# Performance work log

Hardware: AMD Instinct MI355X
Metric: run time of the kernel (lower is better)

Reference implementation:

```python
import jax, jax.numpy as jnp
import numpy as np

N, E, IN = 50000, 800000, 128   # nodes, edges, input feature dim
H, C = 8, 32                    # heads, per-head channels
HC = H * C                      # 256 = concat width
NEG_SLOPE = 0.2
BN_EPS = 1e-5


def _gat_conv(x, src, dst, W, a_src, a_dst, b, heads, out_ch, concat):
    """PyG-style GATConv (eval mode, self-loops already in src/dst)."""
    n = x.shape[0]
    h = (x @ W).reshape(n, heads, out_ch)                 # [N,H,C]
    alpha_s = (h * a_src).sum(-1)                         # [N,H]
    alpha_d = (h * a_dst).sum(-1)                         # [N,H]
    e = jax.nn.leaky_relu(alpha_s[src] + alpha_d[dst], NEG_SLOPE)  # [Etot,H]
    # segment softmax over destination nodes (every node has a self-loop)
    emax = jax.ops.segment_max(e, dst, num_segments=n)    # [N,H]
    e = jnp.exp(e - emax[dst])
    denom = jax.ops.segment_sum(e, dst, num_segments=n)
    alpha = e / (denom[dst] + 1e-16)                      # [Etot,H]
    msg = h[src] * alpha[:, :, None]                      # [Etot,H,C]
    out = jax.ops.segment_sum(msg, dst, num_segments=n)   # [N,H,C]
    out = out.reshape(n, heads * out_ch) if concat else out.mean(axis=1)
    return out + b


def _bn(y, g, beta, m, v):
    return (y - m) * jax.lax.rsqrt(v + BN_EPS) * g + beta


def setup_inputs() -> dict:
    key = jax.random.key(0)
    ks = jax.random.split(key, 32)
    def p(i, shape, s=0.1):
        return jax.random.normal(ks[i], shape, dtype=jnp.float32) * s
    x = jax.random.normal(ks[0], (N, IN), dtype=jnp.float32)
    edge_index = jax.random.randint(ks[1], (2, E), 0, N, dtype=jnp.int32)
    d = dict(
        x=x, edge_index=edge_index,
        W1=p(2, (IN, HC)), a_src1=p(3, (H, C)), a_dst1=p(4, (H, C)), b1=p(5, (HC,)),
        bn1_g=jnp.ones((HC,), jnp.float32), bn1_b=jnp.zeros((HC,), jnp.float32),
        bn1_m=p(6, (HC,)), bn1_v=jax.random.uniform(ks[7], (HC,), jnp.float32, 0.5, 1.5),
        W2=p(8, (HC, HC)), a_src2=p(9, (H, C)), a_dst2=p(10, (H, C)), b2=p(11, (HC,)),
        bn2_g=jnp.ones((HC,), jnp.float32), bn2_b=jnp.zeros((HC,), jnp.float32),
        bn2_m=p(12, (HC,)), bn2_v=jax.random.uniform(ks[13], (HC,), jnp.float32, 0.5, 1.5),
        W3=p(14, (HC, C)), a_src3=p(15, (1, C)), a_dst3=p(16, (1, C)), b3=p(17, (C,)),
        Ws1=p(18, (IN, HC)), bs1=p(19, (HC,)),
        Ws2=p(20, (HC, C)), bs2=p(21, (C,)),
    )
    return d


def reference(x, edge_index, W1, a_src1, a_dst1, b1, bn1_g, bn1_b, bn1_m, bn1_v,
              W2, a_src2, a_dst2, b2, bn2_g, bn2_b, bn2_m, bn2_v,
              W3, a_src3, a_dst3, b3, Ws1, bs1, Ws2, bs2):
    n = x.shape[0]
    loops = jnp.arange(n, dtype=edge_index.dtype)
    src = jnp.concatenate([edge_index[0], loops])   # PyG add_self_loops=True
    dst = jnp.concatenate([edge_index[1], loops])
    x0 = x @ Ws1 + bs1                               # skip1
    h = _gat_conv(x, src, dst, W1, a_src1, a_dst1, b1, H, C, True)
    h = jax.nn.elu(_bn(h, bn1_g, bn1_b, bn1_m, bn1_v)) + x0
    xs = h @ Ws2 + bs2                               # skip2
    h2 = _gat_conv(h, src, dst, W2, a_src2, a_dst2, b2, H, C, True)
    h2 = jax.nn.elu(_bn(h2, bn2_g, bn2_b, bn2_m, bn2_v))
    out = _gat_conv(h2, src, dst, W3, a_src3, a_dst3, b3, 1, C, False) + xs
    return out
```

## Files before the change

kernel.cpp:

```cpp
#include <hip/hip_runtime.h>
#include <hip/hip_bf16.h>

#define NEG_SLOPE 0.2f
#define BN_EPS 1e-5f
#define BSH 8
#define STASH_CAP 6400

typedef __attribute__((ext_vector_type(8))) short bf16x8;
typedef __attribute__((ext_vector_type(4))) float f32x4;
typedef __attribute__((ext_vector_type(2))) float f32x2;

#if defined(__has_builtin)
#if __has_builtin(__builtin_amdgcn_cvt_f32_fp8) && __has_builtin(__builtin_amdgcn_cvt_pk_fp8_f32)
#define HW_FP8 1
#endif
#if __has_builtin(__builtin_amdgcn_cvt_pk_f32_fp8)
#define HW_FP8_PK 1
#endif
#endif

__device__ __forceinline__ float bf2f(unsigned short u) {
    union { unsigned int i; float f; } x;
    x.i = ((unsigned int)u) << 16;
    return x.f;
}
__device__ __forceinline__ unsigned short f2bf(float f) {
    __hip_bfloat16 b = __float2bfloat16(f);
    return *reinterpret_cast<unsigned short*>(&b);
}
__device__ __forceinline__ float lrelu(float v) {
    return v > 0.f ? v : NEG_SLOPE * v;
}
__device__ __forceinline__ void gload_lds16(const void* g, void* l) {
    __builtin_amdgcn_global_load_lds(
        (const __attribute__((address_space(1))) unsigned int*)(g),
        (__attribute__((address_space(3))) unsigned int*)(l),
        16, 0, 0);
}

__device__ __forceinline__ unsigned char f8enc(float f) {
#ifdef HW_FP8
    int p = __builtin_amdgcn_cvt_pk_fp8_f32(f, 0.f, 0, false);
    return (unsigned char)(p & 0xff);
#else
    float a = fabsf(f);
    unsigned int sign = (__float_as_uint(f) >> 31) << 7;
    if (a < 0.0009765625f) return (unsigned char)sign;
    a = fminf(a, 448.f);
    unsigned int bits = __float_as_uint(a);
    int e = (int)((bits >> 23) & 0xff) - 127;
    unsigned int mant = bits & 0x7fffff;
    if (e < -6) {
        int q = (int)(a * 512.f + 0.5f);
        if (q >= 8) return (unsigned char)(sign | 0x08);
        return (unsigned char)(sign | q);
    }
    unsigned int m = mant >> 20;
    unsigned int rem = mant & 0xfffff;
    if (rem > 0x80000 || (rem == 0x80000 && (m & 1))) m++;
    if (m == 8) { m = 0; e++; }
    if (e > 8) { e = 8; m = 6; }
    return (unsigned char)(sign | ((unsigned int)(e + 7) << 3) | m);
#endif
}
template <int SEL>
__device__ __forceinline__ float f8dec(unsigned int w) {
#ifdef HW_FP8
    return __builtin_amdgcn_cvt_f32_fp8(w, SEL);
#else
    unsigned int b = (w >> (SEL * 8)) & 0xff;
    unsigned int s = b >> 7, em = b & 0x7f;
    float mag;
    if (em >= 8) {
        unsigned int bits = (((em >> 3) + 120) << 23) | ((em & 7) << 20);
        mag = __uint_as_float(bits);
    } else {
        mag = (float)em * 0.001953125f;
    }
    return s ? -mag : mag;
#endif
}
__device__ __forceinline__ void fma_f8x4(float we, unsigned int wv, float4& acc) {
#ifdef HW_FP8_PK
    f32x2 lo = __builtin_amdgcn_cvt_pk_f32_fp8((int)wv, false);
    f32x2 hi = __builtin_amdgcn_cvt_pk_f32_fp8((int)wv, true);
    acc.x = fmaf(we, lo[0], acc.x);
    acc.y = fmaf(we, lo[1], acc.y);
    acc.z = fmaf(we, hi[0], acc.z);
    acc.w = fmaf(we, hi[1], acc.w);
#else
    acc.x = fmaf(we, f8dec<0>(wv), acc.x);
    acc.y = fmaf(we, f8dec<1>(wv), acc.y);
    acc.z = fmaf(we, f8dec<2>(wv), acc.z);
    acc.w = fmaf(we, f8dec<3>(wv), acc.w);
#endif
}

__device__ __forceinline__ int block_scan_incl(int v, int t) {
    int lane = t & 63, w = t >> 6;
    int sv = v;
    #pragma unroll
    for (int off = 1; off < 64; off <<= 1) {
        int u = __shfl_up(sv, off);
        if (lane >= off) sv += u;
    }
    __shared__ int ws_[4];
    if (lane == 63) ws_[w] = sv;
    __syncthreads();
    if (t == 0) {
        int a = 0;
        #pragma unroll
        for (int k = 0; k < 4; k++) { int x = ws_[k]; ws_[k] = a; a += x; }
    }
    __syncthreads();
    return sv + ws_[w];
}

__global__ __launch_bounds__(256) void phase1(const int* __restrict__ dstl,
                                              int E, int N, int NB,
                                              int* __restrict__ gHist,
                                              const float* __restrict__ x,
                                              unsigned short* __restrict__ xb, int n4x,
                                              const float* __restrict__ W1,
                                              const float* __restrict__ Ws1,
                                              const float* __restrict__ W2,
                                              const float* __restrict__ Ws2,
                                              const float* __restrict__ W3,
                                              unsigned short* __restrict__ Wcat1,
                                              unsigned short* __restrict__ Wcat2,
                                              unsigned short* __restrict__ W3t) {
    int t = threadIdx.x;
    if (blockIdx.x < 256) {
        __shared__ int h[256];
        h[t] = 0;
        __syncthreads();
        int Etot = E + N;
        for (int i = blockIdx.x * 256 + t; i < Etot; i += 256 * 256) {
            int d = (i < E) ? dstl[i] : (i - E);
            atomicAdd(&h[d >> BSH], 1);
        }
        __syncthreads();
        if (t < NB && h[t]) atomicAdd(&gHist[t], h[t]);
        return;
    }
    int i = (blockIdx.x - 256) * 256 + t;
    if (i < n4x) {
        float4 v = reinterpret_cast<const float4*>(x)[i];
        ushort4 o;
        o.x = f2bf(v.x); o.y = f2bf(v.y); o.z = f2bf(v.z); o.w = f2bf(v.w);
        reinterpret_cast<ushort4*>(xb)[i] = o;
        return;
    }
    int j = i - n4x;
    if (j < 32768) {
        int m = j >> 7, k = j & 127;
        Wcat1[j] = f2bf(W1[k * 256 + m]);
    } else if (j < 65536) {
        int q = j - 32768; int m = q >> 7, k = q & 127;
        Wcat1[32768 + q] = f2bf(Ws1[k * 256 + m]);
    } else if (j < 131072) {
        int q = j - 65536; int m = q >> 8, k = q & 255;
        Wcat2[q] = f2bf(W2[k * 256 + m]);
    } else if (j < 139264) {
        int q = j - 131072; int m = q >> 8, k = q & 255;
        Wcat2[65536 + q] = f2bf(Ws2[k * 32 + m]);
    } else if (j < 147456) {
        int q = j - 139264; int m = q >> 8, k = q & 255;
        W3t[q] = f2bf(W3[k * 32 + m]);
    }
}

__global__ __launch_bounds__(256) void bucket_scatter(const int* __restrict__ srcl,
                                                      const int* __restrict__ dstl,
                                                      int E, int N, int NB,
                                                      const int* __restrict__ gHist,
                                                      int* __restrict__ gCursor,
                                                      unsigned int* __restrict__ bktEdges) {
    __shared__ unsigned int stage[4096];
    __shared__ int lbase[256];
    __shared__ int hist[256];
    __shared__ int bexcl[257];
    __shared__ int curk[256];
    __shared__ int gbase[256];
    int t = threadIdx.x;
    int Etot = E + N;
    int begin = blockIdx.x * 4096;

    int gv = (t < NB) ? gHist[t] : 0;
    int gincl = block_scan_incl(gv, t);
    lbase[t] = gincl - gv;
    __syncthreads();

    hist[t] = 0;
    __syncthreads();

    unsigned int ent[16];
    int eb[16];
    #pragma unroll
    for (int k = 0; k < 16; k++) {
        int i = begin + k * 256 + t;
        if (i < Etot) {
            int s, d;
            if (i < E) { s = srcl[i]; d = dstl[i]; }
            else       { s = d = i - E; }
            eb[k] = d >> BSH;
            ent[k] = ((unsigned int)s << BSH) | (unsigned int)(d & 255);
            atomicAdd(&hist[eb[k]], 1);
        } else eb[k] = -1;
    }
    __syncthreads();

    int v = hist[t];
    int incl = block_scan_incl(v, t);
    bexcl[t] = incl - v;
    curk[t] = incl - v;
    if (t == 255) bexcl[256] = incl;
    __syncthreads();

    #pragma unroll
    for (int k = 0; k < 16; k++) {
        if (eb[k] >= 0) {
            int slot = atomicAdd(&curk[eb[k]], 1);
            stage[slot] = ent[k];
        }
    }
    if (t < NB) {
        int cnt = hist[t];
        gbase[t] = cnt ? (lbase[t] + atomicAdd(&gCursor[t], cnt)) : 0;
    }
    __syncthreads();

    int total = bexcl[256];
    for (int p = t; p < total; p += 256) {
        int lo = 0, hi = NB - 1;
        while (lo < hi) {
            int mid = (lo + hi + 1) >> 1;
            if (bexcl[mid] <= p) lo = mid; else hi = mid - 1;
        }
        bktEdges[gbase[lo] + (p - bexcl[lo])] = stage[p];
    }
}

__global__ __launch_bounds__(256) void bucket_to_csr(const unsigned int* __restrict__ bktEdges,
                                                     const int* __restrict__ gHist,
                                                     int* __restrict__ indptr,
                                                     int* __restrict__ esrc,
                                                     int N, int NB, int Etot) {
    __shared__ int lbase[256];
    __shared__ int nh[256];
    __shared__ int ncur[256];
    __shared__ unsigned int stash[STASH_CAP];
    int b = blockIdx.x, t = threadIdx.x;

    int gv = (t < NB) ? gHist[t] : 0;
    int gincl = block_scan_incl(gv, t);
    lbase[t] = gincl - gv;
    __syncthreads();
    int base = lbase[b];
    int cnt = gHist[b];
    int nodeBase = b << BSH;

    nh[t] = 0;
    __syncthreads();
    for (int p = t; p < cnt; p += 256) {
        unsigned int e = bktEdges[base + p];
        if (p < STASH_CAP) stash[p] = e;
        atomicAdd(&nh[e & 255], 1);
    }
    __syncthreads();
    int v = nh[t];
    int incl = block_scan_incl(v, t);
    int excl = incl - v;
    ncur[t] = excl;
    if (nodeBase + t < N) indptr[nodeBase + t] = base + excl;
    __syncthreads();
    for (int p = t; p < cnt; p += 256) {
        unsigned int e = (p < STASH_CAP) ? stash[p] : bktEdges[base + p];
        int slot = atomicAdd(&ncur[e & 255], 1);
        esrc[base + slot] = (int)(e >> BSH);
    }
    if (b == 0 && t == 0) indptr[N] = Etot;
}

__global__ __launch_bounds__(256) void gemm_tile(const unsigned short* __restrict__ A,
                                                 const unsigned short* __restrict__ Bt,
                                                 unsigned short* __restrict__ outBf,
                                                 unsigned char* __restrict__ outQ,
                                                 unsigned short* __restrict__ outSk,
                                                 const float* __restrict__ biasSk,
                                                 const float* __restrict__ aS,
                                                 const float* __restrict__ aD,
                                                 float* __restrict__ asOut,
                                                 float* __restrict__ adOut,
                                                 int M, int K, int NCtot, int split,
                                                 int ldBf, int ldSk) {
    __shared__ __align__(16) char smem[2][2][8192];
    int t = threadIdx.x;
    int w = t >> 6, lane = t & 63;
    int l16 = lane & 15, quad = lane >> 4;
    int warp_r = w >> 1, warp_c = w & 1;
    int rowBase = blockIdx.y * 128;
    int colBase = blockIdx.x * 128;

    int row_l = t & 127;
    int jchunk = t >> 7;
    int arow_st = rowBase + row_l; if (arow_st >= M) arow_st = M - 1;
    int bcol_st = colBase + row_l; if (bcol_st >= NCtot) bcol_st = NCtot - 1;
    const unsigned short* aRow = A + (size_t)arow_st * K;
    const unsigned short* bRow = Bt + (size_t)bcol_st * K;

    f32x4 acc[4][4];
    #pragma unroll
    for (int i = 0; i < 4; i++)
        #pragma unroll
        for (int j = 0; j < 4; j++) acc[i][j] = (f32x4){0.f, 0.f, 0.f, 0.f};

    auto stage = [&](int buf, int k0) {
        #pragma unroll
        for (int j = 0; j < 2; j++) {
            int chunk = j * 2 + jchunk;
            gload_lds16(aRow + k0 + chunk * 8, &smem[buf][0][(size_t)j * 4096 + (size_t)t * 16]);
            gload_lds16(bRow + k0 + chunk * 8, &smem[buf][1][(size_t)j * 4096 + (size_t)t * 16]);
        }
    };

    stage(0, 0);
    __syncthreads();
    int niter = K >> 5;
    for (int it = 0; it < niter; ++it) {
        if (it + 1 < niter) stage((it + 1) & 1, (it + 1) << 5);
        const char* Ab = &smem[it & 1][0][0];
        const char* Bb = &smem[it & 1][1][0];
        bf16x8 a[4], b[4];
        #pragma unroll
        for (int i = 0; i < 4; i++)
            a[i] = *reinterpret_cast<const bf16x8*>(Ab + quad * 2048 + (warp_r * 64 + i * 16 + l16) * 16);
        #pragma unroll
        for (int j = 0; j < 4; j++)
            b[j] = *reinterpret_cast<const bf16x8*>(Bb + quad * 2048 + (warp_c * 64 + j * 16 + l16) * 16);
        #pragma unroll
        for (int i = 0; i < 4; i++)
            #pragma unroll
            for (int j = 0; j < 4; j++)
                acc[i][j] = __builtin_amdgcn_mfma_f32_16x16x32_bf16(a[i], b[j], acc[i][j], 0, 0, 0);
        __syncthreads();
    }

    if (aS && colBase < split) {
        if (NCtot >= 128) {
            int c0 = colBase + warp_c * 64 + l16;
            int hbase = (colBase + warp_c * 64) >> 5;
            float as0 = aS[c0],      ad0 = aD[c0];
            float as1 = aS[c0 + 16], ad1 = aD[c0 + 16];
            float as2 = aS[c0 + 32], ad2 = aD[c0 + 32];
            float as3 = aS[c0 + 48], ad3 = aD[c0 + 48];
            #pragma unroll
            for (int i = 0; i < 4; i++) {
                #pragma unroll
                for (int r = 0; r < 4; r++) {
                    float va0 = acc[i][0][r] * as0 + acc[i][1][r] * as1;
                    float vd0 = acc[i][0][r] * ad0 + acc[i][1][r] * ad1;
                    float va1 = acc[i][2][r] * as2 + acc[i][3][r] * as3;
                    float vd1 = acc[i][2][r] * ad2 + acc[i][3][r] * ad3;
                    #pragma unroll
                    for (int off = 1; off < 16; off <<= 1) {
                        va0 += __shfl_xor(va0, off);
                        vd0 += __shfl_xor(vd0, off);
                        va1 += __shfl_xor(va1, off);
                        vd1 += __shfl_xor(vd1, off);
                    }
                    int row = rowBase + warp_r * 64 + i * 16 + quad * 4 + r;
                    if (l16 == 0 && row < M) {
                        asOut[row * 8 + hbase]     = va0;
                        adOut[row * 8 + hbase]     = vd0;
                        asOut[row * 8 + hbase + 1] = va1;
                        adOut[row * 8 + hbase + 1] = vd1;
                    }
                }
            }
        } else if (warp_c == 0) {
            float as0 = aS[l16],      ad0 = aD[l16];
            float as1 = aS[l16 + 16], ad1 = aD[l16 + 16];
            #pragma unroll
            for (int i = 0; i < 4; i++) {
                #pragma unroll
                for (int r = 0; r < 4; r++) {
                    float va = acc[i][0][r] * as0 + acc[i][1][r] * as1;
                    float vd = acc[i][0][r] * ad0 + acc[i][1][r] * ad1;
                    #pragma unroll
                    for (int off = 1; off < 16; off <<= 1) {
                        va += __shfl_xor(va, off);
                        vd += __shfl_xor(vd, off);
                    }
                    int row = rowBase + warp_r * 64 + i * 16 + quad * 4 + r;
                    if (l16 == 0 && row < M) {
                        asOut[row] = va;
                        adOut[row] = vd;
                    }
                }
            }
        }
    }

    #pragma unroll
    for (int i = 0; i < 4; i++) {
        #pragma unroll
        for (int r = 0; r < 4; r++) {
            int row = rowBase + warp_r * 64 + i * 16 + quad * 4 + r;
            if (row >= M) continue;
            #pragma unroll
            for (int j = 0; j < 4; j++) {
                int c = colBase + warp_c * 64 + j * 16 + l16;
                if (c >= NCtot) continue;
                float v = acc[i][j][r];
                if (c < split) {
                    if (outBf) outBf[(size_t)row * ldBf + c] = f2bf(v);
                    if (outQ)  outQ[(size_t)row * ldBf + c] = f8enc(v);
                } else {
                    outSk[(size_t)row * ldSk + (c - split)] = f2bf(v + biasSk[c - split]);
                }
            }
        }
    }
}

template <int MODE>
__global__ __launch_bounds__(256) void agg256(const unsigned char* __restrict__ hq,
                                              const float* __restrict__ as,
                                              const float* __restrict__ ad,
                                              const int* __restrict__ indptr,
                                              const int* __restrict__ esrc,
                                              const float* __restrict__ bias,
                                              const float* __restrict__ bn_g,
                                              const float* __restrict__ bn_b,
                                              const float* __restrict__ bn_m,
                                              const float* __restrict__ bn_v,
                                              const unsigned short* __restrict__ skip,
                                              unsigned short* __restrict__ out, int N) {
    int t = threadIdx.x;
    int n = blockIdx.x * 4 + (t >> 6);
    if (n >= N) return;
    int lane = t & 63;
    int e8 = lane >> 3, h8 = lane & 7;
    int g4 = lane >> 4, cl = lane & 15;
    int hd = cl >> 1;
    int start = indptr[n], end = indptr[n + 1];
    int cnt = end - start;

    float adh = ad[n * 8 + h8];
    const unsigned char* hqc = hq + cl * 16;

    float4 acc0 = make_float4(0.f, 0.f, 0.f, 0.f);
    float4 acc1 = make_float4(0.f, 0.f, 0.f, 0.f);
    float4 acc2 = make_float4(0.f, 0.f, 0.f, 0.f);
    float4 acc3 = make_float4(0.f, 0.f, 0.f, 0.f);
    float sm = 0.f;
    int nfull = cnt & ~7;

    int sA = 0, sB = 0;
    float wA = 0.f, wB = 0.f;
    uint4 hv0 = {}, hv1 = {};
    if (nfull) {
        sA = esrc[start + e8];
        wA = __expf(lrelu(as[sA * 8 + h8] + adh));
        int r0 = __shfl(sA, g4 * 8);
        int r1 = __shfl(sA, (4 + g4) * 8);
        hv0 = *reinterpret_cast<const uint4*>(hqc + (size_t)r0 * 256);
        hv1 = *reinterpret_cast<const uint4*>(hqc + (size_t)r1 * 256);
        if (nfull > 8) {
            sB = esrc[start + 8 + e8];
            wB = __expf(lrelu(as[sB * 8 + h8] + adh));
        }
    }
    for (int i0 = start; i0 < start + nfull; i0 += 8) {
        uint4 u0 = hv0, u1 = hv1;
        float wcur = wA;
        if (i0 + 8 < start + nfull) {
            int r0 = __shfl(sB, g4 * 8);
            int r1 = __shfl(sB, (4 + g4) * 8);
            hv0 = *reinterpret_cast<const uint4*>(hqc + (size_t)r0 * 256);
            hv1 = *reinterpret_cast<const uint4*>(hqc + (size_t)r1 * 256);
        }
        sA = sB; wA = wB;
        if (i0 + 16 < start + nfull) {
            sB = esrc[i0 + 16 + e8];
            wB = __expf(lrelu(as[sB * 8 + h8] + adh));
        }
        sm += wcur;
        float w0 = __shfl(wcur, g4 * 8 + hd);
        float w1 = __shfl(wcur, (4 + g4) * 8 + hd);
        fma_f8x4(w0, u0.x, acc0);
        fma_f8x4(w0, u0.y, acc1);
        fma_f8x4(w0, u0.z, acc2);
        fma_f8x4(w0, u0.w, acc3);
        fma_f8x4(w1, u1.x, acc0);
        fma_f8x4(w1, u1.y, acc1);
        fma_f8x4(w1, u1.z, acc2);
        fma_f8x4(w1, u1.w, acc3);
    }
    int rem = cnt - nfull;
    if (rem) {
        int i0 = start + nfull;
        int idx = i0 + e8;
        bool valid = idx < end;
        int s_r = esrc[valid ? idx : end - 1];
        float w_r = valid ? __expf(lrelu(as[s_r * 8 + h8] + adh)) : 0.f;
        sm += w_r;
        int r0 = __shfl(s_r, g4 * 8);
        uint4 u0 = *reinterpret_cast<const uint4*>(hqc + (size_t)r0 * 256);
        float w0 = __shfl(w_r, g4 * 8 + hd);
        fma_f8x4(w0, u0.x, acc0);
        fma_f8x4(w0, u0.y, acc1);
        fma_f8x4(w0, u0.z, acc2);
        fma_f8x4(w0, u0.w, acc3);
        if (rem > 4) {
            int r1 = __shfl(s_r, (4 + g4) * 8);
            uint4 u1 = *reinterpret_cast<const uint4*>(hqc + (size_t)r1 * 256);
            float w1 = __shfl(w_r, (4 + g4) * 8 + hd);
            fma_f8x4(w1, u1.x, acc0);
            fma_f8x4(w1, u1.y, acc1);
            fma_f8x4(w1, u1.z, acc2);
            fma_f8x4(w1, u1.w, acc3);
        }
    }

    acc0.x += __shfl_xor(acc0.x, 16); acc0.y += __shfl_xor(acc0.y, 16);
    acc0.z += __shfl_xor(acc0.z, 16); acc0.w += __shfl_xor(acc0.w, 16);
    acc0.x += __shfl_xor(acc0.x, 32); acc0.y += __shfl_xor(acc0.y, 32);
    acc0.z += __shfl_xor(acc0.z, 32); acc0.w += __shfl_xor(acc0.w, 32);
    acc1.x += __shfl_xor(acc1.x, 16); acc1.y += __shfl_xor(acc1.y, 16);
    acc1.z += __shfl_xor(acc1.z, 16); acc1.w += __shfl_xor(acc1.w, 16);
    acc1.x += __shfl_xor(acc1.x, 32); acc1.y += __shfl_xor(acc1.y, 32);
    acc1.z += __shfl_xor(acc1.z, 32); acc1.w += __shfl_xor(acc1.w, 32);
    acc2.x += __shfl_xor(acc2.x, 16); acc2.y += __shfl_xor(acc2.y, 16);
    acc2.z += __shfl_xor(acc2.z, 16); acc2.w += __shfl_xor(acc2.w, 16);
    acc2.x += __shfl_xor(acc2.x, 32); acc2.y += __shfl_xor(acc2.y, 32);
    acc2.z += __shfl_xor(acc2.z, 32); acc2.w += __shfl_xor(acc2.w, 32);
    acc3.x += __shfl_xor(acc3.x, 16); acc3.y += __shfl_xor(acc3.y, 16);
    acc3.z += __shfl_xor(acc3.z, 16); acc3.w += __shfl_xor(acc3.w, 16);
    acc3.x += __shfl_xor(acc3.x, 32); acc3.y += __shfl_xor(acc3.y, 32);
    acc3.z += __shfl_xor(acc3.z, 32); acc3.w += __shfl_xor(acc3.w, 32);

    #pragma unroll
    for (int off = 8; off < 64; off <<= 1) sm += __shfl_xor(sm, off);
    float il = 1.f / (sm + 1e-16f);
    float il_c = __shfl(il, hd);

    float4 my;
    if (g4 == 0)      my = acc0;
    else if (g4 == 1) my = acc1;
    else if (g4 == 2) my = acc2;
    else              my = acc3;
    int cb = cl * 16 + g4 * 4;

    float4 bv  = *reinterpret_cast<const float4*>(&bias[cb]);
    float4 gv  = *reinterpret_cast<const float4*>(&bn_g[cb]);
    float4 bbv = *reinterpret_cast<const float4*>(&bn_b[cb]);
    float4 mv  = *reinterpret_cast<const float4*>(&bn_m[cb]);
    float4 vv  = *reinterpret_cast<const float4*>(&bn_v[cb]);
    float o[4] = {my.x * il_c + bv.x, my.y * il_c + bv.y,
                  my.z * il_c + bv.z, my.w * il_c + bv.w};
    float g[4] = {gv.x, gv.y, gv.z, gv.w}, bb[4] = {bbv.x, bbv.y, bbv.z, bbv.w};
    float m[4] = {mv.x, mv.y, mv.z, mv.w}, vr[4] = {vv.x, vv.y, vv.z, vv.w};
    float sk[4] = {0.f, 0.f, 0.f, 0.f};
    if (MODE == 1) {
        ushort4 s4 = *reinterpret_cast<const ushort4*>(&skip[(size_t)n * 256 + cb]);
        sk[0] = bf2f(s4.x); sk[1] = bf2f(s4.y); sk[2] = bf2f(s4.z); sk[3] = bf2f(s4.w);
    }
    ushort4 res;
    unsigned short* rp = &res.x;
    #pragma unroll
    for (int j = 0; j < 4; j++) {
        float val = (o[j] - m[j]) * rsqrtf(vr[j] + BN_EPS) * g[j] + bb[j];
        val = val > 0.f ? val : (__expf(val) - 1.f);
        val += sk[j];
        rp[j] = f2bf(val);
    }
    *reinterpret_cast<ushort4*>(&out[(size_t)n * 256 + cb]) = res;
}

__global__ __launch_bounds__(256) void agg32(const unsigned short* __restrict__ h3,
                                             const float* __restrict__ as,
                                             const float* __restrict__ ad,
                                             const int* __restrict__ indptr,
                                             const int* __restrict__ esrc,
                                             const float* __restrict__ b3,
                                             const unsigned short* __restrict__ xs,
                                             float* __restrict__ out, int N) {
    int t = threadIdx.x;
    int n = blockIdx.x * 4 + (t >> 6);
    if (n >= N) return;
    int lane = t & 63;
    int e_sub = lane >> 3, c4 = (lane & 7) * 4;
    int start = indptr[n], end = indptr[n + 1];
    float adn = ad[n];

    float4 acc = make_float4(0.f, 0.f, 0.f, 0.f);
    float sm = 0.f;
    int i0 = start;
    for (; i0 + 16 <= end; i0 += 16) {
        int sA = esrc[i0 + e_sub];
        int sB = esrc[i0 + 8 + e_sub];
        float wA = __expf(lrelu(as[sA] + adn));
        float wB = __expf(lrelu(as[sB] + adn));
        sm += wA + wB;
        ushort4 hA = *reinterpret_cast<const ushort4*>(&h3[(size_t)sA * 32 + c4]);
        ushort4 hB = *reinterpret_cast<const ushort4*>(&h3[(size_t)sB * 32 + c4]);
        acc.x = fmaf(wA, bf2f(hA.x), acc.x); acc.y = fmaf(wA, bf2f(hA.y), acc.y);
        acc.z = fmaf(wA, bf2f(hA.z), acc.z); acc.w = fmaf(wA, bf2f(hA.w), acc.w);
        acc.x = fmaf(wB, bf2f(hB.x), acc.x); acc.y = fmaf(wB, bf2f(hB.y), acc.y);
        acc.z = fmaf(wB, bf2f(hB.z), acc.z); acc.w = fmaf(wB, bf2f(hB.w), acc.w);
    }
    for (; i0 < end; i0 += 8) {
        int idx = i0 + e_sub;
        bool valid = idx < end;
        if (valid) {
            int s = esrc[idx];
            float w = __expf(lrelu(as[s] + adn));
            sm += w;
            ushort4 hv = *reinterpret_cast<const ushort4*>(&h3[(size_t)s * 32 + c4]);
            acc.x = fmaf(w, bf2f(hv.x), acc.x);
            acc.y = fmaf(w, bf2f(hv.y), acc.y);
            acc.z = fmaf(w, bf2f(hv.z), acc.z);
            acc.w = fmaf(w, bf2f(hv.w), acc.w);
        }
    }
    #pragma unroll
    for (int off = 8; off < 64; off <<= 1) {
        sm    += __shfl_xor(sm, off);
        acc.x += __shfl_xor(acc.x, off);
        acc.y += __shfl_xor(acc.y, off);
        acc.z += __shfl_xor(acc.z, off);
        acc.w += __shfl_xor(acc.w, off);
    }
    if (e_sub == 0) {
        float il = 1.f / (sm + 1e-16f);
        float4 bv = *reinterpret_cast<const float4*>(&b3[c4]);
        ushort4 xv = *reinterpret_cast<const ushort4*>(&xs[(size_t)n * 32 + c4]);
        float4 o;
        o.x = acc.x * il + bv.x + bf2f(xv.x);
        o.y = acc.y * il + bv.y + bf2f(xv.y);
        o.z = acc.z * il + bv.z + bf2f(xv.z);
        o.w = acc.w * il + bv.w + bf2f(xv.w);
        *reinterpret_cast<float4*>(&out[(size_t)n * 32 + c4]) = o;
    }
}

extern "C" void kernel_launch(void* const* d_in, const int* in_sizes, int n_in,
                              void* d_out, int out_size, void* d_ws, size_t ws_size,
                              hipStream_t stream) {
    const float* x      = (const float*)d_in[0];
    const int*   eidx   = (const int*)  d_in[1];
    const float* W1     = (const float*)d_in[2];
    const float* a_src1 = (const float*)d_in[3];
    const float* a_dst1 = (const float*)d_in[4];
    const float* b1     = (const float*)d_in[5];
    const float* bn1_g  = (const float*)d_in[6];
    const float* bn1_b  = (const float*)d_in[7];
    const float* bn1_m  = (const float*)d_in[8];
    const float* bn1_v  = (const float*)d_in[9];
    const float* W2     = (const float*)d_in[10];
    const float* a_src2 = (const float*)d_in[11];
    const float* a_dst2 = (const float*)d_in[12];
    const float* b2     = (const float*)d_in[13];
    const float* bn2_g  = (const float*)d_in[14];
    const float* bn2_b  = (const float*)d_in[15];
    const float* bn2_m  = (const float*)d_in[16];
    const float* bn2_v  = (const float*)d_in[17];
    const float* W3     = (const float*)d_in[18];
    const float* a_src3 = (const float*)d_in[19];
    const float* a_dst3 = (const float*)d_in[20];
    const float* b3     = (const float*)d_in[21];
    const float* Ws1    = (const float*)d_in[22];
    const float* bs1    = (const float*)d_in[23];
    const float* Ws2    = (const float*)d_in[24];
    const float* bs2    = (const float*)d_in[25];

    const int N = in_sizes[0] / 128;
    const int E = in_sizes[1] / 2;
    const int Etot = E + N;
    const int NB = (N + 255) >> 8;
    const int* srcl = eidx;
    const int* dstl = eidx + E;

    char* ws = (char*)d_ws;
    size_t off = 0;
    auto alloc = [&](size_t bytes) -> void* {
        void* p = ws + off;
        off += (bytes + 255) & ~(size_t)255;
        return p;
    };
    unsigned short* xb    = (unsigned short*)alloc((size_t)N * 128 * 2);
    unsigned short* feat  = (unsigned short*)alloc((size_t)N * 256 * 2);
    unsigned char*  hq    = (unsigned char*)alloc((size_t)N * 256);
    unsigned short* h2b   = (unsigned short*)alloc((size_t)N * 256 * 2);
    unsigned short* featb = (unsigned short*)alloc((size_t)N * 256 * 2);
    unsigned short* xsbuf = (unsigned short*)alloc((size_t)N * 32 * 2);
    unsigned short* h3b   = (unsigned short*)alloc((size_t)N * 32 * 2);
    float*          asb   = (float*)alloc((size_t)N * 8 * 4);
    float*          adb   = (float*)alloc((size_t)N * 8 * 4);
    unsigned short* Wcat1 = (unsigned short*)alloc((size_t)512 * 128 * 2);
    unsigned short* Wcat2 = (unsigned short*)alloc((size_t)288 * 256 * 2);
    unsigned short* W3t   = (unsigned short*)alloc((size_t)32 * 256 * 2);
    int* gHC     = (int*)alloc(512 * 4);
    int* gHist   = gHC;
    int* gCursor = gHC + 256;
    unsigned int* bktEdges = (unsigned int*)alloc((size_t)Etot * 4);
    int* indptr  = (int*)alloc((size_t)(N + 1) * 4);
    int* esrc    = (int*)alloc((size_t)Etot * 4);
    (void)ws_size; (void)n_in; (void)out_size;

    hipMemsetAsync(gHC, 0, 512 * 4, stream);
    int n4x = N * 128 / 4;
    int prepBlocks = (n4x + 147456 + 255) / 256;
    phase1<<<256 + prepBlocks, 256, 0, stream>>>(dstl, E, N, NB, gHist,
                                                 x, xb, n4x,
                                                 W1, Ws1, W2, Ws2, W3,
                                                 Wcat1, Wcat2, W3t);
    bucket_scatter<<<(Etot + 4095) / 4096, 256, 0, stream>>>(srcl, dstl, E, N, NB,
                                                             gHist, gCursor, bktEdges);
    bucket_to_csr<<<NB, 256, 0, stream>>>(bktEdges, gHist, indptr, esrc, N, NB, Etot);

    int gy128 = (N + 127) / 128;
    int gn4 = (N + 3) / 4;

    gemm_tile<<<dim3(4, gy128), 256, 0, stream>>>(xb, Wcat1, nullptr, hq, feat, bs1,
                                                  a_src1, a_dst1, asb, adb,
                                                  N, 128, 512, 256, 256, 256);
    agg256<1><<<gn4, 256, 0, stream>>>(hq, asb, adb, indptr, esrc, b1,
                                       bn1_g, bn1_b, bn1_m, bn1_v, feat, h2b, N);

    gemm_tile<<<dim3(3, gy128), 256, 0, stream>>>(h2b, Wcat2, nullptr, hq, xsbuf, bs2,
                                                  a_src2, a_dst2, asb, adb,
                                                  N, 256, 288, 256, 256, 32);
    agg256<0><<<gn4, 256, 0, stream>>>(hq, asb, adb, indptr, esrc, b2,
                                       bn2_g, bn2_b, bn2_m, bn2_v, nullptr, featb, N);

    gemm_tile<<<dim3(1, gy128), 256, 0, stream>>>(featb, W3t, h3b, nullptr, h3b, nullptr,
                                                  a_src3, a_dst3, asb, adb,
                                                  N, 256, 32, 32, 32, 32);
    agg32<<<gn4, 256, 0, stream>>>(h3b, asb, adb, indptr, esrc, b3, xsbuf,
                                   (float*)d_out, N);
}
```

Measured before the change: 392.9 us.

## Fold attention vectors into weight matrices as extra GEMM output columns

```diff
diff --git a/kernel.cpp b/kernel.cpp
--- a/kernel.cpp
+++ b/kernel.cpp
@@ -126,6 +126,12 @@
                                               const float* __restrict__ W2,
                                               const float* __restrict__ Ws2,
                                               const float* __restrict__ W3,
+                                              const float* __restrict__ a_src1,
+                                              const float* __restrict__ a_dst1,
+                                              const float* __restrict__ a_src2,
+                                              const float* __restrict__ a_dst2,
+                                              const float* __restrict__ a_src3,
+                                              const float* __restrict__ a_dst3,
                                               unsigned short* __restrict__ Wcat1,
                                               unsigned short* __restrict__ Wcat2,
                                               unsigned short* __restrict__ W3t) {
@@ -167,6 +173,29 @@
     } else if (j < 147456) {
         int q = j - 139264; int m = q >> 8, k = q & 255;
         W3t[q] = f2bf(W3[k * 32 + m]);
+    } else if (j < 149504) {
+        int q = j - 147456; int r = q >> 7, k = q & 127;
+        int h = r & 7;
+        const float* av = (r < 8) ? a_src1 : a_dst1;
+        float s = 0.f;
+        #pragma unroll
+        for (int c = 0; c < 32; c++) s += W1[k * 256 + h * 32 + c] * av[h * 32 + c];
+        Wcat1[(512 + r) * 128 + k] = f2bf(s);
+    } else if (j < 153600) {
+        int q = j - 149504; int r = q >> 8, k = q & 255;
+        int h = r & 7;
+        const float* av = (r < 8) ? a_src2 : a_dst2;
+        float s = 0.f;
+        #pragma unroll
+        for (int c = 0; c < 32; c++) s += W2[k * 256 + h * 32 + c] * av[h * 32 + c];
+        Wcat2[(288 + r) * 256 + k] = f2bf(s);
+    } else if (j < 154112) {
+        int q = j - 153600; int r = q >> 8, k = q & 255;
+        const float* av = r ? a_dst3 : a_src3;
+        float s = 0.f;
+        #pragma unroll
+        for (int c = 0; c < 32; c++) s += W3[k * 32 + c] * av[c];
+        W3t[(32 + r) * 256 + k] = f2bf(s);
     }
 }
 
@@ -288,11 +317,10 @@
                                                  unsigned char* __restrict__ outQ,
                                                  unsigned short* __restrict__ outSk,
                                                  const float* __restrict__ biasSk,
-                                                 const float* __restrict__ aS,
-                                                 const float* __restrict__ aD,
                                                  float* __restrict__ asOut,
                                                  float* __restrict__ adOut,
-                                                 int M, int K, int NCtot, int split,
+                                                 int M, int K, int NCtot,
+                                                 int split, int split2,
                                                  int ldBf, int ldSk) {
     __shared__ __align__(16) char smem[2][2][8192];
     int t = threadIdx.x;
@@ -344,62 +372,6 @@
             for (int j = 0; j < 4; j++)
                 acc[i][j] = __builtin_amdgcn_mfma_f32_16x16x32_bf16(a[i], b[j], acc[i][j], 0, 0, 0);
         __syncthreads();
-    }
-
-    if (aS && colBase < split) {
-        if (NCtot >= 128) {
-            int c0 = colBase + warp_c * 64 + l16;
-            int hbase = (colBase + warp_c * 64) >> 5;
-            float as0 = aS[c0],      ad0 = aD[c0];
-            float as1 = aS[c0 + 16], ad1 = aD[c0 + 16];
-            float as2 = aS[c0 + 32], ad2 = aD[c0 + 32];
-            float as3 = aS[c0 + 48], ad3 = aD[c0 + 48];
-            #pragma unroll
-            for (int i = 0; i < 4; i++) {
-                #pragma unroll
-                for (int r = 0; r < 4; r++) {
-                    float va0 = acc[i][0][r] * as0 + acc[i][1][r] * as1;
-                    float vd0 = acc[i][0][r] * ad0 + acc[i][1][r] * ad1;
-                    float va1 = acc[i][2][r] * as2 + acc[i][3][r] * as3;
-                    float vd1 = acc[i][2][r] * ad2 + acc[i][3][r] * ad3;
-                    #pragma unroll
-                    for (int off = 1; off < 16; off <<= 1) {
-                        va0 += __shfl_xor(va0, off);
-                        vd0 += __shfl_xor(vd0, off);
-                        va1 += __shfl_xor(va1, off);
-                        vd1 += __shfl_xor(vd1, off);
-                    }
-                    int row = rowBase + warp_r * 64 + i * 16 + quad * 4 + r;
-                    if (l16 == 0 && row < M) {
-                        asOut[row * 8 + hbase]     = va0;
-                        adOut[row * 8 + hbase]     = vd0;
-                        asOut[row * 8 + hbase + 1] = va1;
-                        adOut[row * 8 + hbase + 1] = vd1;
-                    }
-                }
-            }
-        } else if (warp_c == 0) {
-            float as0 = aS[l16],      ad0 = aD[l16];
-            float as1 = aS[l16 + 16], ad1 = aD[l16 + 16];
-            #pragma unroll
-            for (int i = 0; i < 4; i++) {
-                #pragma unroll
-                for (int r = 0; r < 4; r++) {
-                    float va = acc[i][0][r] * as0 + acc[i][1][r] * as1;
-                    float vd = acc[i][0][r] * ad0 + acc[i][1][r] * ad1;
-                    #pragma unroll
-                    for (int off = 1; off < 16; off <<= 1) {
-                        va += __shfl_xor(va, off);
-                        vd += __shfl_xor(vd, off);
-                    }
-                    int row = rowBase + warp_r * 64 + i * 16 + quad * 4 + r;
-                    if (l16 == 0 && row < M) {
-                        asOut[row] = va;
-                        adOut[row] = vd;
-                    }
-                }
-            }
-        }
     }
 
     #pragma unroll
@@ -416,8 +388,17 @@
                 if (c < split) {
                     if (outBf) outBf[(size_t)row * ldBf + c] = f2bf(v);
                     if (outQ)  outQ[(size_t)row * ldBf + c] = f8enc(v);
+                } else if (c < split2) {
+                    outSk[(size_t)row * ldSk + (c - split)] = f2bf(v + biasSk[c - split]);
                 } else {
-                    outSk[(size_t)row * ldSk + (c - split)] = f2bf(v + biasSk[c - split]);
+                    int a = c - split2;
+                    if (NCtot - split2 == 16) {
+                        if (a < 8) asOut[(size_t)row * 8 + a] = v;
+                        else       adOut[(size_t)row * 8 + a - 8] = v;
+                    } else {
+                        if (a == 0) asOut[row] = v;
+                        else        adOut[row] = v;
+                    }
                 }
             }
         }
@@ -699,9 +680,9 @@
     unsigned short* h3b   = (unsigned short*)alloc((size_t)N * 32 * 2);
     float*          asb   = (float*)alloc((size_t)N * 8 * 4);
     float*          adb   = (float*)alloc((size_t)N * 8 * 4);
-    unsigned short* Wcat1 = (unsigned short*)alloc((size_t)512 * 128 * 2);
-    unsigned short* Wcat2 = (unsigned short*)alloc((size_t)288 * 256 * 2);
-    unsigned short* W3t   = (unsigned short*)alloc((size_t)32 * 256 * 2);
+    unsigned short* Wcat1 = (unsigned short*)alloc((size_t)528 * 128 * 2);
+    unsigned short* Wcat2 = (unsigned short*)alloc((size_t)304 * 256 * 2);
+    unsigned short* W3t   = (unsigned short*)alloc((size_t)34 * 256 * 2);
     int* gHC     = (int*)alloc(512 * 4);
     int* gHist   = gHC;
     int* gCursor = gHC + 256;
@@ -712,10 +693,12 @@
 
     hipMemsetAsync(gHC, 0, 512 * 4, stream);
     int n4x = N * 128 / 4;
-    int prepBlocks = (n4x + 147456 + 255) / 256;
+    int prepBlocks = (n4x + 154112 + 255) / 256;
     phase1<<<256 + prepBlocks, 256, 0, stream>>>(dstl, E, N, NB, gHist,
                                                  x, xb, n4x,
                                                  W1, Ws1, W2, Ws2, W3,
+                                                 a_src1, a_dst1, a_src2, a_dst2,
+                                                 a_src3, a_dst3,
                                                  Wcat1, Wcat2, W3t);
     bucket_scatter<<<(Etot + 4095) / 4096, 256, 0, stream>>>(srcl, dstl, E, N, NB,
                                                              gHist, gCursor, bktEdges);
@@ -724,21 +707,21 @@
     int gy128 = (N + 127) / 128;
     int gn4 = (N + 3) / 4;
 
-    gemm_tile<<<dim3(4, gy128), 256, 0, stream>>>(xb, Wcat1, nullptr, hq, feat, bs1,
-                                                  a_src1, a_dst1, asb, adb,
-                                                  N, 128, 512, 256, 256, 256);
+    gemm_tile<<<dim3(5, gy128), 256, 0, stream>>>(xb, Wcat1, nullptr, hq, feat, bs1,
+                                                  asb, adb,
+                                                  N, 128, 528, 256, 512, 256, 256);
     agg256<1><<<gn4, 256, 0, stream>>>(hq, asb, adb, indptr, esrc, b1,
                                        bn1_g, bn1_b, bn1_m, bn1_v, feat, h2b, N);
 
     gemm_tile<<<dim3(3, gy128), 256, 0, stream>>>(h2b, Wcat2, nullptr, hq, xsbuf, bs2,
-                                                  a_src2, a_dst2, asb, adb,
-                                                  N, 256, 288, 256, 256, 32);
+                                                  asb, adb,
+                                                  N, 256, 304, 256, 288, 256, 32);
     agg256<0><<<gn4, 256, 0, stream>>>(hq, asb, adb, indptr, esrc, b2,
                                        bn2_g, bn2_b, bn2_m, bn2_v, nullptr, featb, N);
 
-    gemm_tile<<<dim3(1, gy128), 256, 0, stream>>>(featb, W3t, h3b, nullptr, h3b, nullptr,
-                                                  a_src3, a_dst3, asb, adb,
-                                                  N, 256, 32, 32, 32, 32);
+    gemm_tile<<<dim3(1, gy128), 256, 0, stream>>>(featb, W3t, h3b, nullptr, nullptr, nullptr,
+                                                  asb, adb,
+                                                  N, 256, 34, 32, 32, 32, 32);
     agg32<<<gn4, 256, 0, stream>>>(h3b, asb, adb, indptr, esrc, b3, xsbuf,
                                    (float*)d_out, N);
 }
```

Result: faster. 383.9 us (-2.3%).
